# Optimization experiments

Hardware: AMD Instinct MI355X
Metric: run time of the kernel (lower is better)

## Reference

```python
import jax, jax.numpy as jnp
import numpy as np

N, F_IN, F_OUT = 20000, 512, 512
E = 320000
S = 6           # max_subgraph_size
T = 0.5         # evolution_time
HSCALE = 0.05   # Hamiltonian scale
MAX_TERMS = 4   # truncated matrix-exp series terms
EPS = 1e-5      # BatchNorm eps


def _build_subgraphs(edge_index_np):
    # deterministic stand-in for SubgraphCache: 1-hop in-neighbors, center first,
    # truncated to S nodes (matches mapping=0 after subsampling in the original)
    loops = np.stack([np.arange(N), np.arange(N)])
    ei = np.concatenate([edge_index_np.astype(np.int64), loops], axis=1)
    codes = np.unique(ei[0] * N + ei[1])   # dedup directed edges incl. self loops
    src, dst = codes // N, codes % N
    order = np.argsort(dst, kind='stable')
    src_s, dst_s = src[order], dst[order]
    starts = np.searchsorted(dst_s, np.arange(N))
    ends = np.searchsorted(dst_s, np.arange(N) + 1)
    sub_nodes = np.zeros((N, S), dtype=np.int32)
    valid = np.zeros((N, S), dtype=bool)
    for i in range(N):
        nb = np.unique(src_s[starts[i]:ends[i]])
        nb = nb[nb != i][:S - 1]
        k = 1 + nb.shape[0]
        sub_nodes[i, 0] = i
        sub_nodes[i, 1:k] = nb
        valid[i, :k] = True
    # induced directed adjacency of each size-S subgraph (padded slots zeroed)
    pair = sub_nodes[:, :, None].astype(np.int64) * N + sub_nodes[:, None, :].astype(np.int64)
    hit = np.isin(pair, codes)
    pv = valid[:, :, None] & valid[:, None, :]
    sub_adj = (hit & pv).astype(np.int32)
    return jnp.asarray(sub_nodes), jnp.asarray(sub_adj)


def setup_inputs() -> dict:
    key = jax.random.key(0)
    ks = jax.random.split(key, 4)
    x = jax.random.normal(ks[0], (N, F_IN), dtype=jnp.float32)
    edge_index = jax.random.randint(ks[1], (2, E), 0, N, dtype=jnp.int32)
    sub_nodes, sub_adj = _build_subgraphs(np.asarray(edge_index))
    W_re = jax.random.normal(ks[2], (F_IN, F_OUT), dtype=jnp.float32) * 0.02
    W_im = jax.random.normal(ks[3], (F_IN, F_OUT), dtype=jnp.float32) * 0.02
    b_re = jnp.zeros((F_OUT,), jnp.float32)
    b_im = jnp.zeros((F_OUT,), jnp.float32)
    gamma_r = jnp.ones((F_OUT,), jnp.float32)
    beta_r = jnp.zeros((F_OUT,), jnp.float32)
    gamma_i = jnp.ones((F_OUT,), jnp.float32)
    beta_i = jnp.zeros((F_OUT,), jnp.float32)
    return {"x": x, "edge_index": edge_index, "sub_nodes": sub_nodes,
            "sub_adj": sub_adj, "W_re": W_re, "W_im": W_im, "b_re": b_re,
            "b_im": b_im, "gamma_r": gamma_r, "beta_r": beta_r,
            "gamma_i": gamma_i, "beta_i": beta_i}


def _bn(v, gamma, beta):
    # training-mode BatchNorm1d (biased variance), applied per real/imag part
    mu = v.mean(axis=0)
    var = jnp.var(v, axis=0)
    return (v - mu) * jax.lax.rsqrt(var + EPS) * gamma + beta


def reference(x, edge_index, sub_nodes, sub_adj, W_re, W_im, b_re, b_im,
              gamma_r, beta_r, gamma_i, beta_i):
    # ComplexLinear on real-valued input: y = x @ (W_re + i W_im) + b
    y = jax.lax.complex(x @ W_re + b_re, x @ W_im + b_im)    # [N, F_OUT] c64
    # per-node subgraph Laplacian Hamiltonian: L = diag(deg) - A, H = 0.05 * L
    A = sub_adj.astype(jnp.float32)                          # [N, S, S]
    deg = A.sum(-1)                                          # degree(row)
    L = deg[:, :, None] * jnp.eye(S, dtype=jnp.float32) - A
    scaled = (-1j * T * HSCALE) * L.astype(jnp.complex64)    # -i * H * t
    # center row (index 0) of truncated series exp(-iHt); lower block of the
    # 2dim unitary hits zero-padded z rows, so only U_sub row 0 matters
    v = jnp.zeros((N, S), jnp.complex64).at[:, 0].set(1.0)
    term, res = v, v
    for k in range(1, MAX_TERMS + 1):
        term = jnp.einsum('ns,nst->nt', term, scaled) / k
        res = res + term
    sub_x = y[sub_nodes]                                     # [N, S, F_OUT]
    evolved = jnp.einsum('ns,nsf->nf', res, sub_x)           # center of U @ z
    # complex ReLU -> naive complex BatchNorm -> residual (in==out, no proj)
    er, ei = jax.nn.relu(evolved.real), jax.nn.relu(evolved.imag)
    out_r = _bn(er, gamma_r, beta_r) + x
    out_i = _bn(ei, gamma_i, beta_i)
    # complex output represented as concat(real, imag)
    return jnp.concatenate([out_r, out_i], axis=-1)          # [N, 2*F_OUT]
```

## Files before the change

### kernel.cpp

```cpp
#include <hip/hip_runtime.h>

#define N_NODES 20000
#define FDIM 512
#define SSZ 6

typedef __attribute__((ext_vector_type(8))) short bf16x8;
typedef __attribute__((ext_vector_type(4))) float f32x4;
typedef __attribute__((ext_vector_type(8))) unsigned short u16x8;

static __device__ __forceinline__ unsigned short f2bf(float f) {
    unsigned int u = __float_as_uint(f);
    unsigned int r = (u + 0x7fffu + ((u >> 16) & 1u)) >> 16;
    return (unsigned short)r;
}
static __device__ __forceinline__ float bf2f(unsigned short u) {
    return __uint_as_float(((unsigned int)u) << 16);
}

__global__ __launch_bounds__(256) void conv_all(
    const float* __restrict__ x, const float* __restrict__ Wre,
    const float* __restrict__ Wim, unsigned short* __restrict__ xb,
    unsigned short* __restrict__ wt, float* __restrict__ sums)
{
    const int blk = blockIdx.x;
    const int tid = threadIdx.x;
    if (blk < 5000) {
        const size_t i = ((size_t)blk * 256 + tid) * 8;
        const float4 a = *(const float4*)(x + i);
        const float4 b = *(const float4*)(x + i + 4);
        u16x8 o;
        o[0] = f2bf(a.x); o[1] = f2bf(a.y); o[2] = f2bf(a.z); o[3] = f2bf(a.w);
        o[4] = f2bf(b.x); o[5] = f2bf(b.y); o[6] = f2bf(b.z); o[7] = f2bf(b.w);
        *(u16x8*)(xb + i) = o;
    } else if (blk < 5512) {
        __shared__ float tile[32][33];
        const int bidx = blk - 5000;
        const int z = bidx >> 8;
        const int rem = bidx & 255;
        const int k0 = (rem & 15) * 32;
        const int n0 = (rem >> 4) * 32;
        const float* W = z ? Wim : Wre;
        const int tx = tid & 31, ty = tid >> 5;
#pragma unroll
        for (int i = 0; i < 4; ++i)
            tile[ty + i * 8][tx] = W[(size_t)(k0 + ty + i * 8) * FDIM + n0 + tx];
        __syncthreads();
        unsigned short* wtb = wt + (size_t)z * FDIM * FDIM;
#pragma unroll
        for (int i = 0; i < 4; ++i)
            wtb[(size_t)(n0 + ty + i * 8) * FDIM + k0 + tx] = f2bf(tile[tx][ty + i * 8]);
    } else {
#pragma unroll
        for (int i = 0; i < 8; ++i) sums[i * 256 + tid] = 0.f;
    }
}

#define BM 64
#define BN 128
#define BK 64

__global__ __launch_bounds__(256) void gemm_mfma(
    const unsigned short* __restrict__ xb,
    const unsigned short* __restrict__ wt,
    const float* __restrict__ bre, const float* __restrict__ bim,
    unsigned short* __restrict__ y)
{
    __shared__ __align__(16) unsigned short lA[BM * BK];
    __shared__ __align__(16) unsigned short lB[BN * BK];

    const int tid  = threadIdx.x;
    const int wave = tid >> 6;
    const int lane = tid & 63;
    const int rowBase = blockIdx.y * BM;
    const int colBase = blockIdx.x * BN;

    const int wm = (wave >> 1) * 32;
    const int wn = (wave & 1) * 64;

    f32x4 acc[2][4];
#pragma unroll
    for (int i = 0; i < 2; ++i)
#pragma unroll
        for (int j = 0; j < 4; ++j) acc[i][j] = (f32x4){0.f, 0.f, 0.f, 0.f};

    const int srow   = lane >> 3;
    const int schunk = lane & 7;
    const int gchunk = schunk ^ srow;

    const int fm = lane & 15;
    const int kq = lane >> 4;

    for (int k0 = 0; k0 < FDIM; k0 += BK) {
#pragma unroll
        for (int i = 0; i < 2; ++i) {
            const int trow = wave * 16 + i * 8;
            int grow = rowBase + trow + srow;
            if (grow > N_NODES - 1) grow = N_NODES - 1;
            const unsigned short* gp = xb + (size_t)grow * FDIM + k0 + gchunk * 8;
            __builtin_amdgcn_global_load_lds(
                (const __attribute__((address_space(1))) void*)gp,
                (__attribute__((address_space(3))) void*)(lA + trow * BK), 16, 0, 0);
        }
#pragma unroll
        for (int i = 0; i < 4; ++i) {
            const int trow = wave * 32 + i * 8;
            const int grow = colBase + trow + srow;
            const unsigned short* gp = wt + (size_t)grow * FDIM + k0 + gchunk * 8;
            __builtin_amdgcn_global_load_lds(
                (const __attribute__((address_space(1))) void*)gp,
                (__attribute__((address_space(3))) void*)(lB + trow * BK), 16, 0, 0);
        }
        __syncthreads();

#pragma unroll
        for (int ks = 0; ks < 2; ++ks) {
            bf16x8 af[2], bfr[4];
            const int g = ks * 4 + kq;
#pragma unroll
            for (int mt = 0; mt < 2; ++mt) {
                const int row = wm + mt * 16 + fm;
                af[mt] = *(const bf16x8*)&lA[row * BK + ((g ^ (row & 7)) << 3)];
            }
#pragma unroll
            for (int nt = 0; nt < 4; ++nt) {
                const int row = wn + nt * 16 + fm;
                bfr[nt] = *(const bf16x8*)&lB[row * BK + ((g ^ (row & 7)) << 3)];
            }
#pragma unroll
            for (int mt = 0; mt < 2; ++mt)
#pragma unroll
                for (int nt = 0; nt < 4; ++nt)
                    acc[mt][nt] = __builtin_amdgcn_mfma_f32_16x16x32_bf16(
                        af[mt], bfr[nt], acc[mt][nt], 0, 0, 0);
        }
        __syncthreads();
    }

    const int rquad = lane >> 4;
#pragma unroll
    for (int nt = 0; nt < 4; ++nt) {
        const int col = colBase + wn + nt * 16 + fm;
        const float bias = (col < FDIM) ? bre[col] : bim[col - FDIM];
#pragma unroll
        for (int mt = 0; mt < 2; ++mt) {
            const int row0 = rowBase + wm + mt * 16 + rquad * 4;
#pragma unroll
            for (int r = 0; r < 4; ++r) {
                const int row = row0 + r;
                if (row < N_NODES)
                    y[(size_t)row * 1024 + col] = f2bf(acc[mt][nt][r] + bias);
            }
        }
    }
}

__global__ __launch_bounds__(256) void coef_kernel(
    const int* __restrict__ sub_adj, float* __restrict__ coeff)
{
    const int n = blockIdx.x * 256 + threadIdx.x;
    if (n >= N_NODES) return;

    const int* sa = sub_adj + (size_t)n * (SSZ * SSZ);
    float A[SSZ][SSZ], deg[SSZ];
#pragma unroll
    for (int s = 0; s < SSZ; ++s) {
        float d = 0.f;
#pragma unroll
        for (int t = 0; t < SSZ; ++t) { float a = (float)sa[s * SSZ + t]; A[s][t] = a; d += a; }
        deg[s] = d;
    }
    float p1[SSZ], p2[SSZ], p3[SSZ], p4[SSZ];
#pragma unroll
    for (int t = 0; t < SSZ; ++t) p1[t] = ((t == 0) ? deg[0] : 0.f) - A[0][t];
#pragma unroll
    for (int t = 0; t < SSZ; ++t) {
        float acc = 0.f;
#pragma unroll
        for (int s = 0; s < SSZ; ++s) acc += p1[s] * (((s == t) ? deg[s] : 0.f) - A[s][t]);
        p2[t] = acc;
    }
#pragma unroll
    for (int t = 0; t < SSZ; ++t) {
        float acc = 0.f;
#pragma unroll
        for (int s = 0; s < SSZ; ++s) acc += p2[s] * (((s == t) ? deg[s] : 0.f) - A[s][t]);
        p3[t] = acc;
    }
#pragma unroll
    for (int t = 0; t < SSZ; ++t) {
        float acc = 0.f;
#pragma unroll
        for (int s = 0; s < SSZ; ++s) acc += p3[s] * (((s == t) ? deg[s] : 0.f) - A[s][t]);
        p4[t] = acc;
    }
    float rre[SSZ], rim[SSZ];
#pragma unroll
    for (int t = 0; t < SSZ; ++t) {
        rre[t] = ((t == 0) ? 1.f : 0.f) - 3.125e-4f * p2[t] + 1.6276041666666668e-8f * p4[t];
        rim[t] = -0.025f * p1[t] + 2.6041666666666666e-6f * p3[t];
    }

    float* cf = coeff + (size_t)n * 12;
    *(float4*)(cf)     = make_float4(rre[0], rre[1], rre[2], rre[3]);
    *(float4*)(cf + 4) = make_float4(rre[4], rre[5], rim[0], rim[1]);
    *(float4*)(cf + 8) = make_float4(rim[2], rim[3], rim[4], rim[5]);
}

__global__ __launch_bounds__(256) void evolve_stats(
    const unsigned short* __restrict__ y,
    const int* __restrict__ sub_nodes,
    const float* __restrict__ coeff,
    unsigned short* __restrict__ eb,
    float* __restrict__ sums)
{
    __shared__ float lsum[2048];
    const int wave = threadIdx.x >> 6;
    const int lane = threadIdx.x & 63;
    const int f = lane << 3;

    float sR[8] = {0.f}, sR2[8] = {0.f}, sI[8] = {0.f}, sI2[8] = {0.f};

#pragma unroll 1
    for (int q = 0; q < 2; ++q) {
        const int n = blockIdx.x * 8 + wave * 2 + q;

        const float* cf = coeff + (size_t)n * 12;
        const float4 c0 = *(const float4*)(cf);
        const float4 c1 = *(const float4*)(cf + 4);
        const float4 c2 = *(const float4*)(cf + 8);
        const float rre[SSZ] = {c0.x, c0.y, c0.z, c0.w, c1.x, c1.y};
        const float rim[SSZ] = {c1.z, c1.w, c2.x, c2.y, c2.z, c2.w};

        float aR[8] = {0.f}, aI[8] = {0.f};
#pragma unroll
        for (int s = 0; s < SSZ; ++s) {
            const int nd = sub_nodes[n * SSZ + s];
            const float cr = rre[s], ci = rim[s];
            const unsigned short* base = y + (size_t)nd * 1024 + f;
            const u16x8 yr8 = *(const u16x8*)base;
            const u16x8 yi8 = *(const u16x8*)(base + FDIM);
#pragma unroll
            for (int j = 0; j < 8; ++j) {
                const float yr = bf2f(yr8[j]);
                const float yi = bf2f(yi8[j]);
                aR[j] = fmaf(cr, yr, fmaf(-ci, yi, aR[j]));
                aI[j] = fmaf(cr, yi, fmaf(ci, yr, aI[j]));
            }
        }
        u16x8 er8, ei8;
#pragma unroll
        for (int j = 0; j < 8; ++j) {
            const unsigned short re = f2bf(fmaxf(aR[j], 0.f));
            const unsigned short im = f2bf(fmaxf(aI[j], 0.f));
            er8[j] = re; ei8[j] = im;
            const float erv = bf2f(re), eiv = bf2f(im);
            sR[j] += erv;  sR2[j] = fmaf(erv, erv, sR2[j]);
            sI[j] += eiv;  sI2[j] = fmaf(eiv, eiv, sI2[j]);
        }
        *(u16x8*)(eb + (size_t)n * 1024 + f) = er8;
        *(u16x8*)(eb + (size_t)n * 1024 + FDIM + f) = ei8;
    }

    if (wave == 0) {
#pragma unroll
        for (int j = 0; j < 8; ++j) {
            lsum[f + j] = sR[j];  lsum[512 + f + j] = sR2[j];
            lsum[1024 + f + j] = sI[j];  lsum[1536 + f + j] = sI2[j];
        }
    }
    for (int w = 1; w < 4; ++w) {
        __syncthreads();
        if (wave == w) {
#pragma unroll
            for (int j = 0; j < 8; ++j) {
                lsum[f + j] += sR[j];  lsum[512 + f + j] += sR2[j];
                lsum[1024 + f + j] += sI[j];  lsum[1536 + f + j] += sI2[j];
            }
        }
    }
    __syncthreads();
#pragma unroll
    for (int i = 0; i < 8; ++i) {
        const int idx = i * 256 + threadIdx.x;
        atomicAdd(&sums[idx], lsum[idx]);
    }
}

__global__ __launch_bounds__(256) void finalize_kernel(
    const float* __restrict__ x, const unsigned short* __restrict__ eb,
    const float* __restrict__ sums,
    const float* __restrict__ gr, const float* __restrict__ br_,
    const float* __restrict__ gi, const float* __restrict__ bi_,
    float* __restrict__ out)
{
    const int gid = blockIdx.x * 256 + threadIdx.x;
    const int n = gid >> 6;
    const int f = (gid & 63) << 3;
    const float invN = 1.0f / (float)N_NODES;

    float scr[8], shr[8], sci[8], shi[8];
#pragma unroll
    for (int h = 0; h < 2; ++h) {
        const int fo = f + h * 4;
        const float4 s1 = *(const float4*)(sums + fo);
        const float4 s2 = *(const float4*)(sums + 512 + fo);
        const float4 s3 = *(const float4*)(sums + 1024 + fo);
        const float4 s4 = *(const float4*)(sums + 1536 + fo);
        const float4 g1 = *(const float4*)(gr + fo);
        const float4 b1 = *(const float4*)(br_ + fo);
        const float4 g2 = *(const float4*)(gi + fo);
        const float4 b2 = *(const float4*)(bi_ + fo);
        const float mu[4] = {s1.x * invN, s1.y * invN, s1.z * invN, s1.w * invN};
        const float q2[4] = {s2.x * invN, s2.y * invN, s2.z * invN, s2.w * invN};
        const float mi[4] = {s3.x * invN, s3.y * invN, s3.z * invN, s3.w * invN};
        const float qi[4] = {s4.x * invN, s4.y * invN, s4.z * invN, s4.w * invN};
        const float gg1[4] = {g1.x, g1.y, g1.z, g1.w};
        const float bb1[4] = {b1.x, b1.y, b1.z, b1.w};
        const float gg2[4] = {g2.x, g2.y, g2.z, g2.w};
        const float bb2[4] = {b2.x, b2.y, b2.z, b2.w};
#pragma unroll
        for (int j = 0; j < 4; ++j) {
            const float vr = fmaf(-mu[j], mu[j], q2[j]);
            const float sc1 = rsqrtf(vr + 1e-5f) * gg1[j];
            scr[h * 4 + j] = sc1;
            shr[h * 4 + j] = fmaf(-mu[j], sc1, bb1[j]);
            const float vi = fmaf(-mi[j], mi[j], qi[j]);
            const float sc2 = rsqrtf(vi + 1e-5f) * gg2[j];
            sci[h * 4 + j] = sc2;
            shi[h * 4 + j] = fmaf(-mi[j], sc2, bb2[j]);
        }
    }

    const u16x8 er8 = *(const u16x8*)(eb + (size_t)n * 1024 + f);
    const u16x8 ei8 = *(const u16x8*)(eb + (size_t)n * 1024 + FDIM + f);
    float orr[8], oii[8];
#pragma unroll
    for (int j = 0; j < 8; ++j) {
        const float xv = x[(size_t)n * FDIM + f + j];
        orr[j] = fmaf(bf2f(er8[j]), scr[j], shr[j]) + xv;
        oii[j] = fmaf(bf2f(ei8[j]), sci[j], shi[j]);
    }
#pragma unroll
    for (int j = 0; j < 8; j += 4) {
        *(float4*)(out + (size_t)n * 1024 + f + j) =
            make_float4(orr[j], orr[j + 1], orr[j + 2], orr[j + 3]);
        *(float4*)(out + (size_t)n * 1024 + FDIM + f + j) =
            make_float4(oii[j], oii[j + 1], oii[j + 2], oii[j + 3]);
    }
}

extern "C" void kernel_launch(void* const* d_in, const int* in_sizes, int n_in,
                              void* d_out, int out_size, void* d_ws, size_t ws_size,
                              hipStream_t stream)
{
    const float* x        = (const float*)d_in[0];
    const int* sub_nodes  = (const int*)d_in[2];
    const int* sub_adj    = (const int*)d_in[3];
    const float* Wre      = (const float*)d_in[4];
    const float* Wim      = (const float*)d_in[5];
    const float* bre      = (const float*)d_in[6];
    const float* bim      = (const float*)d_in[7];
    const float* gr       = (const float*)d_in[8];
    const float* br_      = (const float*)d_in[9];
    const float* gi       = (const float*)d_in[10];
    const float* bi_      = (const float*)d_in[11];
    float* out = (float*)d_out;

    unsigned short* y  = (unsigned short*)d_ws;
    unsigned short* eb = y + (size_t)N_NODES * 1024;
    unsigned short* xb = eb + (size_t)N_NODES * 1024;
    unsigned short* wt = xb + (size_t)N_NODES * FDIM;
    float* sums        = (float*)(wt + (size_t)1024 * FDIM);

    float* coeff = (float*)wt;

    conv_all<<<5513, 256, 0, stream>>>(x, Wre, Wim, xb, wt, sums);

    dim3 gg(1024 / BN, (N_NODES + BM - 1) / BM);
    gemm_mfma<<<gg, 256, 0, stream>>>(xb, wt, bre, bim, y);

    coef_kernel<<<(N_NODES + 255) / 256, 256, 0, stream>>>(sub_adj, coeff);

    evolve_stats<<<N_NODES / 8, 256, 0, stream>>>(y, sub_nodes, coeff, eb, sums);

    finalize_kernel<<<(N_NODES * 64) / 256, 256, 0, stream>>>(
        x, eb, sums, gr, br_, gi, bi_, out);
}
```

Before: 286.4 us.

## Enlarge GEMM M-tile and split BatchNorm stats into separate reduction kernel

Doubles the GEMM row tile from 64 to 128 so each wave computes a 64x64 output with more MFMA work per LDS fetch. Separately, the evolve kernel no longer accumulates BatchNorm sums; a new stats kernel re-reads the evolved bf16 buffer in 100-row chunks and does far fewer atomics. This trades an extra pass over the evolved data and an extra launch for less LDS serialization and fewer atomics in the evolve step. The larger tile also raises register pressure and gives the GEMM fewer blocks.

```diff
diff --git a/kernel.cpp b/kernel.cpp
--- a/kernel.cpp
+++ b/kernel.cpp
@@ -55,7 +55,7 @@
     }
 }
 
-#define BM 64
+#define BM 128
 #define BN 128
 #define BK 64
 
@@ -74,12 +74,12 @@
     const int rowBase = blockIdx.y * BM;
     const int colBase = blockIdx.x * BN;
 
-    const int wm = (wave >> 1) * 32;
+    const int wm = (wave >> 1) * 64;
     const int wn = (wave & 1) * 64;
 
-    f32x4 acc[2][4];
-#pragma unroll
-    for (int i = 0; i < 2; ++i)
+    f32x4 acc[4][4];
+#pragma unroll
+    for (int i = 0; i < 4; ++i)
 #pragma unroll
         for (int j = 0; j < 4; ++j) acc[i][j] = (f32x4){0.f, 0.f, 0.f, 0.f};
 
@@ -92,8 +92,8 @@
 
     for (int k0 = 0; k0 < FDIM; k0 += BK) {
 #pragma unroll
-        for (int i = 0; i < 2; ++i) {
-            const int trow = wave * 16 + i * 8;
+        for (int i = 0; i < 4; ++i) {
+            const int trow = wave * 32 + i * 8;
             int grow = rowBase + trow + srow;
             if (grow > N_NODES - 1) grow = N_NODES - 1;
             const unsigned short* gp = xb + (size_t)grow * FDIM + k0 + gchunk * 8;
@@ -114,10 +114,10 @@
 
 #pragma unroll
         for (int ks = 0; ks < 2; ++ks) {
-            bf16x8 af[2], bfr[4];
+            bf16x8 af[4], bfr[4];
             const int g = ks * 4 + kq;
 #pragma unroll
-            for (int mt = 0; mt < 2; ++mt) {
+            for (int mt = 0; mt < 4; ++mt) {
                 const int row = wm + mt * 16 + fm;
                 af[mt] = *(const bf16x8*)&lA[row * BK + ((g ^ (row & 7)) << 3)];
             }
@@ -127,7 +127,7 @@
                 bfr[nt] = *(const bf16x8*)&lB[row * BK + ((g ^ (row & 7)) << 3)];
             }
 #pragma unroll
-            for (int mt = 0; mt < 2; ++mt)
+            for (int mt = 0; mt < 4; ++mt)
 #pragma unroll
                 for (int nt = 0; nt < 4; ++nt)
                     acc[mt][nt] = __builtin_amdgcn_mfma_f32_16x16x32_bf16(
@@ -142,7 +142,7 @@
         const int col = colBase + wn + nt * 16 + fm;
         const float bias = (col < FDIM) ? bre[col] : bim[col - FDIM];
 #pragma unroll
-        for (int mt = 0; mt < 2; ++mt) {
+        for (int mt = 0; mt < 4; ++mt) {
             const int row0 = rowBase + wm + mt * 16 + rquad * 4;
 #pragma unroll
             for (int r = 0; r < 4; ++r) {
@@ -206,19 +206,15 @@
     *(float4*)(cf + 8) = make_float4(rim[2], rim[3], rim[4], rim[5]);
 }
 
-__global__ __launch_bounds__(256) void evolve_stats(
+__global__ __launch_bounds__(256) void evolve_kernel(
     const unsigned short* __restrict__ y,
     const int* __restrict__ sub_nodes,
     const float* __restrict__ coeff,
-    unsigned short* __restrict__ eb,
-    float* __restrict__ sums)
-{
-    __shared__ float lsum[2048];
+    unsigned short* __restrict__ eb)
+{
     const int wave = threadIdx.x >> 6;
     const int lane = threadIdx.x & 63;
     const int f = lane << 3;
-
-    float sR[8] = {0.f}, sR2[8] = {0.f}, sI[8] = {0.f}, sI2[8] = {0.f};
 
 #pragma unroll 1
     for (int q = 0; q < 2; ++q) {
@@ -250,39 +246,54 @@
         u16x8 er8, ei8;
 #pragma unroll
         for (int j = 0; j < 8; ++j) {
-            const unsigned short re = f2bf(fmaxf(aR[j], 0.f));
-            const unsigned short im = f2bf(fmaxf(aI[j], 0.f));
-            er8[j] = re; ei8[j] = im;
-            const float erv = bf2f(re), eiv = bf2f(im);
-            sR[j] += erv;  sR2[j] = fmaf(erv, erv, sR2[j]);
-            sI[j] += eiv;  sI2[j] = fmaf(eiv, eiv, sI2[j]);
+            er8[j] = f2bf(fmaxf(aR[j], 0.f));
+            ei8[j] = f2bf(fmaxf(aI[j], 0.f));
         }
         *(u16x8*)(eb + (size_t)n * 1024 + f) = er8;
         *(u16x8*)(eb + (size_t)n * 1024 + FDIM + f) = ei8;
     }
-
-    if (wave == 0) {
+}
+
+#define SROWS 100
+
+__global__ __launch_bounds__(256) void stats_kernel(
+    const unsigned short* __restrict__ eb, float* __restrict__ sums)
+{
+    __shared__ float ls[2][1024], ls2[2][1024];
+    const int tid  = threadIdx.x;
+    const int colg = tid & 127;
+    const int rh   = tid >> 7;
+    const int c    = colg << 3;
+
+    float s[8] = {0.f}, s2[8] = {0.f};
+    const int r0 = blockIdx.x * SROWS;
+#pragma unroll 2
+    for (int r = r0 + rh; r < r0 + SROWS; r += 2) {
+        const u16x8 v = *(const u16x8*)(eb + (size_t)r * 1024 + c);
 #pragma unroll
         for (int j = 0; j < 8; ++j) {
-            lsum[f + j] = sR[j];  lsum[512 + f + j] = sR2[j];
-            lsum[1024 + f + j] = sI[j];  lsum[1536 + f + j] = sI2[j];
-        }
-    }
-    for (int w = 1; w < 4; ++w) {
-        __syncthreads();
-        if (wave == w) {
-#pragma unroll
-            for (int j = 0; j < 8; ++j) {
-                lsum[f + j] += sR[j];  lsum[512 + f + j] += sR2[j];
-                lsum[1024 + f + j] += sI[j];  lsum[1536 + f + j] += sI2[j];
+            const float xv = bf2f(v[j]);
+            s[j] += xv;
+            s2[j] = fmaf(xv, xv, s2[j]);
+        }
+    }
+#pragma unroll
+    for (int j = 0; j < 8; ++j) { ls[rh][c + j] = s[j]; ls2[rh][c + j] = s2[j]; }
+    __syncthreads();
+    if (rh == 0) {
+#pragma unroll
+        for (int j = 0; j < 8; ++j) {
+            const float a = s[j] + ls[1][c + j];
+            const float b = s2[j] + ls2[1][c + j];
+            const int cc = c + j;
+            if (cc < 512) {
+                atomicAdd(&sums[cc], a);
+                atomicAdd(&sums[cc + 512], b);
+            } else {
+                atomicAdd(&sums[cc + 512], a);
+                atomicAdd(&sums[cc + 1024], b);
             }
         }
-    }
-    __syncthreads();
-#pragma unroll
-    for (int i = 0; i < 8; ++i) {
-        const int idx = i * 256 + threadIdx.x;
-        atomicAdd(&sums[idx], lsum[idx]);
     }
 }
 
@@ -381,7 +392,9 @@
 
     coef_kernel<<<(N_NODES + 255) / 256, 256, 0, stream>>>(sub_adj, coeff);
 
-    evolve_stats<<<N_NODES / 8, 256, 0, stream>>>(y, sub_nodes, coeff, eb, sums);
+    evolve_kernel<<<N_NODES / 8, 256, 0, stream>>>(y, sub_nodes, coeff, eb);
+
+    stats_kernel<<<N_NODES / SROWS, 256, 0, stream>>>(eb, sums);
 
     finalize_kernel<<<(N_NODES * 64) / 256, 256, 0, stream>>>(
         x, eb, sums, gr, br_, gi, bi_, out);
```

Measured after the change: 296.4 us. +3.5%, slower.
